# Kernel optimization log

Hardware: AMD Instinct MI355X
Metric: run time of the kernel (lower is better)

## Reference

```python
import jax, jax.numpy as jnp
import numpy as np

B, F, S = 64, 128, 2048
K_LIST = [8, 4, 2]  # c**i for i in range(k,0,-1) with k=3, c=2
EPS = 1e-5


def setup_inputs() -> dict:
    key = jax.random.key(0)
    ks = jax.random.split(key, 16)
    d = {}
    d["x"] = jax.random.normal(ks[0], (B, F, S), dtype=jnp.float32)
    # BatchNorm1d(seq_len*feature_num) affine params (train-mode batch stats)
    d["bn_gamma"] = jnp.ones((F * S,), jnp.float32)
    d["bn_beta"] = jnp.zeros((F * S,), jnp.float32)
    i = 1
    for s, k in enumerate(K_LIST):
        L = S // k
        d[f"selw1_{s}"] = (jax.random.normal(ks[i], (3 * F, 64), jnp.float32) / np.sqrt(3 * F)).astype(jnp.float32); i += 1
        d[f"selb1_{s}"] = jnp.zeros((64,), jnp.float32)
        d[f"selw2_{s}"] = (jax.random.normal(ks[i], (64, 1), jnp.float32) / 8.0).astype(jnp.float32); i += 1
        d[f"selb2_{s}"] = jnp.zeros((1,), jnp.float32)
        d[f"linw1_{s}"] = (jax.random.normal(ks[i], (L, L), jnp.float32) / np.sqrt(L)).astype(jnp.float32); i += 1
        d[f"linb1_{s}"] = jnp.zeros((L,), jnp.float32)
        d[f"linw2_{s}"] = (jax.random.normal(ks[i], (L, 2 * L), jnp.float32) / np.sqrt(L)).astype(jnp.float32); i += 1
        d[f"linb2_{s}"] = jnp.zeros((2 * L,), jnp.float32)
    return d


def _forward(x, bn_gamma, bn_beta, sel, lin):
    Bx, Fx, Sx = x.shape
    # BatchNorm1d over flattened [B, F*S] channels, training-mode batch stats (biased var)
    xf = x.reshape(Bx, -1)
    mu = xf.mean(axis=0)
    var = xf.var(axis=0)
    xf = (xf - mu) * jax.lax.rsqrt(var + EPS) * bn_gamma + bn_beta
    x = xf.reshape(Bx, Fx, Sx)

    samples = []
    for s, k in enumerate(K_LIST):
        L = Sx // k
        xr = x.reshape(Bx, Fx, L, k)           # non-overlapping windows (kernel==stride)
        avg = xr.mean(axis=-1)                 # AvgPool1d  [B, F, L]
        mx = xr.max(axis=-1)                   # MaxPool1d  [B, F, L]
        pfs = 0.5 * (avg + mx)
        stats = jnp.concatenate(
            [pfs.mean(axis=-1), pfs.std(axis=-1, ddof=1), pfs.max(axis=-1)], axis=1
        )                                      # [B, 3F]
        w1, b1, w2, b2 = sel[s]
        w = jax.nn.sigmoid(jax.nn.relu(stats @ w1 + b1) @ w2 + b2)  # [B, 1] (dropout is eval/identity)
        w = w[:, :, None]                      # [B, 1, 1]
        samples.append(w * avg + (1.0 - w) * mx)
    samples.append(x)

    for s in range(len(K_LIST)):
        lw1, lb1, lw2, lb2 = lin[s]
        h = jax.nn.gelu(samples[s] @ lw1 + lb1, approximate=False)
        samples[s + 1] = samples[s + 1] + h @ lw2 + lb2
    return samples[-1]


def reference(x, bn_gamma, bn_beta,
              selw1_0, selb1_0, selw2_0, selb2_0, linw1_0, linb1_0, linw2_0, linb2_0,
              selw1_1, selb1_1, selw2_1, selb2_1, linw1_1, linb1_1, linw2_1, linb2_1,
              selw1_2, selb1_2, selw2_2, selb2_2, linw1_2, linb1_2, linw2_2, linb2_2):
    sel = [(selw1_0, selb1_0, selw2_0, selb2_0),
           (selw1_1, selb1_1, selw2_1, selb2_1),
           (selw1_2, selb1_2, selw2_2, selb2_2)]
    lin = [(linw1_0, linb1_0, linw2_0, linb2_0),
           (linw1_1, linb1_1, linw2_1, linb2_1),
           (linw1_2, linb1_2, linw2_2, linb2_2)]
    return _forward(x, bn_gamma, bn_beta, sel, lin)
```

## Files before the change

kernel.cpp:

```cpp
#include <hip/hip_runtime.h>
#include <hip/hip_bf16.h>
#include <math.h>

#define B_ 64
#define F_ 128
#define S_ 2048
#define FS_ (F_*S_)
#define M_  (B_*F_)
#define EPS_ 1e-5f

typedef __bf16 v8bf __attribute__((ext_vector_type(8)));
typedef float  v16f __attribute__((ext_vector_type(16)));

__device__ __forceinline__ unsigned short f2bf_rne(float f) {
  unsigned int u = __float_as_uint(f);
  u += 0x7FFF + ((u >> 16) & 1);
  return (unsigned short)(u >> 16);
}
__device__ __forceinline__ float b2f(unsigned short u) {
  return __uint_as_float(((unsigned int)u) << 16);
}
__device__ __forceinline__ unsigned int pack2(float a, float b) {
  return (unsigned int)f2bf_rne(a) | ((unsigned int)f2bf_rne(b) << 16);
}

__device__ __forceinline__ float gelu_exact(float x) {
  return 0.5f * x * (1.0f + erff(x * 0.70710678118654752f));
}

#define GLDS16(g, l) __builtin_amdgcn_global_load_lds( \
    (const __attribute__((address_space(1))) unsigned int*)(g), \
    (__attribute__((address_space(3))) unsigned int*)(l), 16, 0, 0)

__global__ __launch_bounds__(256) void bn_stats_k(const float* __restrict__ x,
    const float* __restrict__ gamma, const float* __restrict__ beta,
    float* __restrict__ scl, float* __restrict__ shf)
{
  int j4 = blockIdx.x * 256 + threadIdx.x;
  const float4* x4 = (const float4*)x;
  float sum[4] = {0,0,0,0}, sq[4] = {0,0,0,0};
  for (int b = 0; b < B_; b++) {
    float4 v = x4[(size_t)b * (FS_/4) + j4];
    float vv[4] = {v.x, v.y, v.z, v.w};
    #pragma unroll
    for (int i = 0; i < 4; i++) { sum[i] += vv[i]; sq[i] += vv[i]*vv[i]; }
  }
  #pragma unroll
  for (int i = 0; i < 4; i++) {
    int j = j4*4 + i;
    float mu  = sum[i] * (1.0f/B_);
    float var = sq[i] * (1.0f/B_) - mu*mu;
    float rstd = rsqrtf(var + EPS_);
    float g = gamma[j];
    scl[j] = rstd * g;
    shf[j] = beta[j] - mu * rstd * g;
  }
}

__global__ __launch_bounds__(256) void bnpool_k(const float* __restrict__ x,
    const float* __restrict__ scl, const float* __restrict__ shf,
    unsigned short* __restrict__ xnb, float* __restrict__ stats)
{
  int bf = blockIdx.x, t = threadIdx.x;
  int b = bf >> 7, f = bf & 127;
  const float4* xp  = (const float4*)(x   + (size_t)bf * S_);
  const float4* scp = (const float4*)(scl + (size_t)f  * S_);
  const float4* shp = (const float4*)(shf + (size_t)f  * S_);

  float xr[8];
  #pragma unroll
  for (int h = 0; h < 2; h++) {
    int i4 = t*2 + h;
    float4 v = xp[i4], sc = scp[i4], sh = shp[i4];
    xr[h*4+0] = fmaf(v.x, sc.x, sh.x);
    xr[h*4+1] = fmaf(v.y, sc.y, sh.y);
    xr[h*4+2] = fmaf(v.z, sc.z, sh.z);
    xr[h*4+3] = fmaf(v.w, sc.w, sh.w);
  }
  uint4 pk;
  pk.x = pack2(xr[0], xr[1]); pk.y = pack2(xr[2], xr[3]);
  pk.z = pack2(xr[4], xr[5]); pk.w = pack2(xr[6], xr[7]);
  ((uint4*)(xnb + (size_t)bf * S_))[t] = pk;

  float a2[4], m2[4];
  float ps2 = 0.f, pq2 = 0.f, pm2 = -INFINITY;
  #pragma unroll
  for (int j = 0; j < 4; j++) {
    a2[j] = xr[2*j] + xr[2*j+1];
    m2[j] = fmaxf(xr[2*j], xr[2*j+1]);
    float pf = 0.5f * (0.5f * a2[j] + m2[j]);
    ps2 += pf; pq2 += pf*pf; pm2 = fmaxf(pm2, pf);
  }
  float a4[2], m4[2];
  float ps1 = 0.f, pq1 = 0.f, pm1 = -INFINITY;
  #pragma unroll
  for (int j = 0; j < 2; j++) {
    a4[j] = a2[2*j] + a2[2*j+1];
    m4[j] = fmaxf(m2[2*j], m2[2*j+1]);
    float pf = 0.5f * (0.25f * a4[j] + m4[j]);
    ps1 += pf; pq1 += pf*pf; pm1 = fmaxf(pm1, pf);
  }
  float a8 = a4[0] + a4[1];
  float m8 = fmaxf(m4[0], m4[1]);
  float pf8 = 0.5f * (0.125f * a8 + m8);
  float ps0 = pf8, pq0 = pf8*pf8, pm0 = pf8;

  __shared__ float wred[12];
  int lane = t & 63, wid = t >> 6;
  float PS[3] = {ps0, ps1, ps2}, PQ[3] = {pq0, pq1, pq2}, PM[3] = {pm0, pm1, pm2};
  int   LL[3] = {256, 512, 1024};
  #pragma unroll
  for (int s = 0; s < 3; s++) {
    float vs = PS[s], vq = PQ[s], vm = PM[s];
    #pragma unroll
    for (int off = 32; off > 0; off >>= 1) {
      vs += __shfl_down(vs, off);
      vq += __shfl_down(vq, off);
      vm = fmaxf(vm, __shfl_down(vm, off));
    }
    if (lane == 0) { wred[wid*3+0] = vs; wred[wid*3+1] = vq; wred[wid*3+2] = vm; }
    __syncthreads();
    if (t == 0) {
      float S = 0.f, Q = 0.f, Mx = -INFINITY;
      #pragma unroll
      for (int i = 0; i < 4; i++) {
        S += wred[i*3+0]; Q += wred[i*3+1]; Mx = fmaxf(Mx, wred[i*3+2]);
      }
      float L = (float)LL[s];
      float mean = S / L;
      float var  = (Q - S*S/L) / (L - 1.0f);
      float* base = stats + s*(64*384) + b*384;
      base[f]       = mean;
      base[128 + f] = sqrtf(fmaxf(var, 0.0f));
      base[256 + f] = Mx;
    }
    __syncthreads();
  }
}

__global__ __launch_bounds__(64) void selall_k(const float* __restrict__ stats,
    const float* w1_0, const float* b1_0, const float* w2_0, const float* b2_0,
    const float* w1_1, const float* b1_1, const float* w2_1, const float* b2_1,
    const float* w1_2, const float* b1_2, const float* w2_2, const float* b2_2,
    float* __restrict__ wsel)
{
  int s = blockIdx.y, b = blockIdx.x, j = threadIdx.x;
  const float *w1, *b1, *w2, *b2;
  if      (s == 0) { w1 = w1_0; b1 = b1_0; w2 = w2_0; b2 = b2_0; }
  else if (s == 1) { w1 = w1_1; b1 = b1_1; w2 = w2_1; b2 = b2_1; }
  else             { w1 = w1_2; b1 = b1_2; w2 = w2_2; b2 = b2_2; }
  const float* st = stats + s*(64*384) + b*384;
  float acc = b1[j];
  for (int i = 0; i < 384; i++) acc = fmaf(st[i], w1[i*64 + j], acc);
  float h = fmaxf(acc, 0.0f);
  float v = h * w2[j];
  for (int off = 32; off > 0; off >>= 1) v += __shfl_down(v, off);
  if (j == 0) wsel[s*64 + b] = 1.0f / (1.0f + expf(-(v + b2[0])));
}

__global__ __launch_bounds__(256) void combfused_k(const unsigned short* __restrict__ xnb,
    const float* __restrict__ wsel,
    unsigned short* __restrict__ o8, unsigned short* __restrict__ o4,
    unsigned short* __restrict__ o2)
{
  int bf = blockIdx.x, t = threadIdx.x, b = bf >> 7;
  float wA = wsel[b];
  float wB = wsel[64 + b];
  float wC = wsel[128 + b];
  uint4 pk = ((const uint4*)(xnb + (size_t)bf * S_))[t];
  unsigned int pw[4] = {pk.x, pk.y, pk.z, pk.w};
  float xr[8];
  #pragma unroll
  for (int h = 0; h < 4; h++) {
    xr[2*h]   = b2f((unsigned short)(pw[h] & 0xFFFF));
    xr[2*h+1] = b2f((unsigned short)(pw[h] >> 16));
  }
  float a2[4], m2[4];
  ushort4 u4o;
  unsigned short uu[4];
  #pragma unroll
  for (int j = 0; j < 4; j++) {
    a2[j] = xr[2*j] + xr[2*j+1];
    m2[j] = fmaxf(xr[2*j], xr[2*j+1]);
    uu[j] = f2bf_rne(wC * (0.5f * a2[j]) + (1.0f - wC) * m2[j]);
  }
  u4o.x = uu[0]; u4o.y = uu[1]; u4o.z = uu[2]; u4o.w = uu[3];
  ((ushort4*)(o2 + (size_t)bf * 1024))[t] = u4o;

  float a4[2], m4[2];
  ushort2 u2o;
  #pragma unroll
  for (int j = 0; j < 2; j++) {
    a4[j] = a2[2*j] + a2[2*j+1];
    m4[j] = fmaxf(m2[2*j], m2[2*j+1]);
    unsigned short uv = f2bf_rne(wB * (0.25f * a4[j]) + (1.0f - wB) * m4[j]);
    if (j == 0) u2o.x = uv; else u2o.y = uv;
  }
  ((ushort2*)(o4 + (size_t)bf * 512))[t] = u2o;

  float a8 = a4[0] + a4[1];
  float m8 = fmaxf(m4[0], m4[1]);
  o8[(size_t)bf * 256 + t] = f2bf_rne(wA * (0.125f * a8) + (1.0f - wA) * m8);
}

__global__ __launch_bounds__(256) void wt_all_k(
    const float* w10, unsigned short* t10,
    const float* w20, unsigned short* t20,
    const float* w11, unsigned short* t11,
    const float* w21, unsigned short* t21,
    const float* w12, unsigned short* t12,
    const float* w22, unsigned short* t22)
{
  int bx = blockIdx.x;
  const float* W; unsigned short* T; int K, N, loc;
  if      (bx < 64)   { W = w10; T = t10; K = 256;  N = 256;  loc = bx; }
  else if (bx < 192)  { W = w20; T = t20; K = 256;  N = 512;  loc = bx - 64; }
  else if (bx < 448)  { W = w11; T = t11; K = 512;  N = 512;  loc = bx - 192; }
  else if (bx < 960)  { W = w21; T = t21; K = 512;  N = 1024; loc = bx - 448; }
  else if (bx < 1984) { W = w12; T = t12; K = 1024; N = 1024; loc = bx - 960; }
  else                { W = w22; T = t22; K = 1024; N = 2048; loc = bx - 1984; }
  int nx = N >> 5;
  int k0 = (loc / nx) << 5;
  int n0 = (loc % nx) << 5;
  __shared__ float tile[32][33];
  int tx = threadIdx.x & 31, ty = threadIdx.x >> 5;
  #pragma unroll
  for (int i = ty; i < 32; i += 8)
    tile[i][tx] = W[(size_t)(k0 + i) * N + n0 + tx];
  __syncthreads();
  #pragma unroll
  for (int i = ty; i < 32; i += 8)
    T[(size_t)(n0 + i) * K + k0 + tx] = f2bf_rne(tile[tx][i]);
}

template<int MODE, int TM>
__global__ __launch_bounds__(256) void mgemm_k(
    const unsigned short* __restrict__ A,
    const unsigned short* __restrict__ Wt,
    const float* __restrict__ bias,
    const unsigned short* Cold,
    unsigned short* Obf,
    float* Of32,
    int K, int N)
{
  constexpr int MI = TM / 64;
  constexpr int RA = TM / 4;
  __shared__ v8bf As8[TM * 8];
  __shared__ v8bf Bs8[128 * 8];
  const int tid  = threadIdx.x;
  const int lane = tid & 63;
  const int w    = tid >> 6;
  const int bm   = blockIdx.y * TM;
  const int bn   = blockIdx.x * 128;
  const int wm   = (w >> 1) * (TM / 2);
  const int wn   = (w & 1) * 64;

  v16f acc[MI][2];
  #pragma unroll
  for (int i = 0; i < MI; i++)
    #pragma unroll
    for (int j = 0; j < 2; j++)
      #pragma unroll
      for (int r = 0; r < 16; r++) acc[i][j][r] = 0.f;

  const int lrow = lane >> 3;
  const int lchk = (lane & 7) ^ lrow;
  const unsigned short* ag = A  + (size_t)(bm + w*RA + lrow) * K + lchk * 8;
  const unsigned short* bg = Wt + (size_t)(bn + w*32 + lrow) * K + lchk * 8;
  char* al = (char*)As8 + w*RA*128;
  char* bl = (char*)Bs8 + w*32*128;
  const size_t row8 = (size_t)8 * K;

  for (int k0 = 0; k0 < K; k0 += 64) {
    __syncthreads();
    #pragma unroll
    for (int q = 0; q < RA/8; q++)
      GLDS16(ag + q*row8 + k0, al + q*8*128);
    #pragma unroll
    for (int q = 0; q < 4; q++)
      GLDS16(bg + q*row8 + k0, bl + q*8*128);
    __syncthreads();

    #pragma unroll
    for (int s = 0; s < 4; s++) {
      const int c = 2*s + (lane >> 5);
      const int slot = c ^ (lane & 7);
      v8bf af[MI], bfr[2];
      #pragma unroll
      for (int i = 0; i < MI; i++)
        af[i] = As8[(wm + i*32 + (lane & 31))*8 + slot];
      #pragma unroll
      for (int j = 0; j < 2; j++)
        bfr[j] = Bs8[(wn + j*32 + (lane & 31))*8 + slot];
      #pragma unroll
      for (int i = 0; i < MI; i++)
        #pragma unroll
        for (int j = 0; j < 2; j++)
          acc[i][j] = __builtin_amdgcn_mfma_f32_32x32x16_bf16(af[i], bfr[j], acc[i][j], 0, 0, 0);
    }
  }

  const int col0 = bn + wn + (lane & 31);
  const int rb0  = bm + wm + ((lane >> 5) << 2);
  #pragma unroll
  for (int j = 0; j < 2; j++) {
    int c = col0 + j*32;
    float bv = bias[c];
    #pragma unroll
    for (int i = 0; i < MI; i++) {
      #pragma unroll
      for (int r = 0; r < 16; r++) {
        int rr = rb0 + i*32 + (r & 3) + ((r >> 2) << 3);
        size_t idx = (size_t)rr * N + c;
        float t = acc[i][j][r] + bv;
        if (MODE == 0) {
          Obf[idx] = f2bf_rne(gelu_exact(t));
        } else if (MODE == 1) {
          Obf[idx] = f2bf_rne(t + b2f(Cold[idx]));
        } else {
          Of32[idx] = t + b2f(Cold[idx]);
        }
      }
    }
  }
}

extern "C" void kernel_launch(void* const* d_in, const int* in_sizes, int n_in,
                              void* d_out, int out_size, void* d_ws, size_t ws_size,
                              hipStream_t stream)
{
  const float* x     = (const float*)d_in[0];
  const float* gamma = (const float*)d_in[1];
  const float* beta  = (const float*)d_in[2];
  float* out = (float*)d_out;
  float* ws  = (float*)d_ws;

  static const int KS[3] = {8, 4, 2};

  size_t off = 0;
  float* scl   = ws + off; off += FS_;
  float* shf   = ws + off; off += FS_;
  float* stats = ws + off; off += 3*64*384;
  float* wsel  = ws + off; off += 256;
  unsigned short* xnb = (unsigned short*)(ws + off); off += (size_t)M_ * S_ / 2;
  unsigned short* sampb[3];
  sampb[0] = (unsigned short*)(ws + off); off += (size_t)M_ * 256 / 2;
  sampb[1] = (unsigned short*)(ws + off); off += (size_t)M_ * 512 / 2;
  sampb[2] = (unsigned short*)(ws + off); off += (size_t)M_ * 1024 / 2;
  unsigned short* hb = (unsigned short*)(ws + off); off += (size_t)M_ * 2048 / 2;
  unsigned short *wt1[3], *wt2[3];
  for (int s = 0; s < 3; s++) {
    int L = S_ / KS[s];
    wt1[s] = (unsigned short*)(ws + off); off += (size_t)L * L / 2;
    wt2[s] = (unsigned short*)(ws + off); off += (size_t)L * 2 * L / 2;
  }

  wt_all_k<<<4032, 256, 0, stream>>>(
      (const float*)d_in[3 + 0*8 + 4], wt1[0], (const float*)d_in[3 + 0*8 + 6], wt2[0],
      (const float*)d_in[3 + 1*8 + 4], wt1[1], (const float*)d_in[3 + 1*8 + 6], wt2[1],
      (const float*)d_in[3 + 2*8 + 4], wt1[2], (const float*)d_in[3 + 2*8 + 6], wt2[2]);

  bn_stats_k<<<FS_/4/256, 256, 0, stream>>>(x, gamma, beta, scl, shf);
  bnpool_k<<<M_, 256, 0, stream>>>(x, scl, shf, xnb, stats);
  selall_k<<<dim3(64, 3), 64, 0, stream>>>(stats,
      (const float*)d_in[3+0], (const float*)d_in[4+0], (const float*)d_in[5+0], (const float*)d_in[6+0],
      (const float*)d_in[3+8], (const float*)d_in[4+8], (const float*)d_in[5+8], (const float*)d_in[6+8],
      (const float*)d_in[3+16], (const float*)d_in[4+16], (const float*)d_in[5+16], (const float*)d_in[6+16],
      wsel);
  combfused_k<<<M_, 256, 0, stream>>>(xnb, wsel, sampb[0], sampb[1], sampb[2]);

  mgemm_k<0,64><<<dim3(2, 128), 256, 0, stream>>>(
      sampb[0], wt1[0], (const float*)d_in[3+0*8+5], nullptr, hb, nullptr, 256, 256);
  mgemm_k<1,64><<<dim3(4, 128), 256, 0, stream>>>(
      hb, wt2[0], (const float*)d_in[3+0*8+7], sampb[1], sampb[1], nullptr, 256, 512);
  mgemm_k<0,64><<<dim3(4, 128), 256, 0, stream>>>(
      sampb[1], wt1[1], (const float*)d_in[3+1*8+5], nullptr, hb, nullptr, 512, 512);
  mgemm_k<1,64><<<dim3(8, 128), 256, 0, stream>>>(
      hb, wt2[1], (const float*)d_in[3+1*8+7], sampb[2], sampb[2], nullptr, 512, 1024);
  mgemm_k<0,64><<<dim3(8, 128), 256, 0, stream>>>(
      sampb[2], wt1[2], (const float*)d_in[3+2*8+5], nullptr, hb, nullptr, 1024, 1024);
  mgemm_k<2,128><<<dim3(16, 64), 256, 0, stream>>>(
      hb, wt2[2], (const float*)d_in[3+2*8+7], xnb, nullptr, out, 1024, 2048);
}
```

Measured before the change: 372.0 us.

## Prefetch next GEMM K-tile into registers while computing current tile

Replaces the direct global-to-LDS loads in the bf16 MFMA GEMM with register prefetching. The next K-tile is loaded into registers while the MFMAs run on the current tile, then written to LDS after a barrier. This aims to hide global memory latency behind compute without adding LDS buffers. The cost is extra VGPR pressure and a register round-trip for the data.

```diff
diff --git a/kernel.cpp b/kernel.cpp
--- a/kernel.cpp
+++ b/kernel.cpp
@@ -27,10 +27,6 @@
 __device__ __forceinline__ float gelu_exact(float x) {
   return 0.5f * x * (1.0f + erff(x * 0.70710678118654752f));
 }
-
-#define GLDS16(g, l) __builtin_amdgcn_global_load_lds( \
-    (const __attribute__((address_space(1))) unsigned int*)(g), \
-    (__attribute__((address_space(3))) unsigned int*)(l), 16, 0, 0)
 
 __global__ __launch_bounds__(256) void bn_stats_k(const float* __restrict__ x,
     const float* __restrict__ gamma, const float* __restrict__ beta,
@@ -245,6 +241,7 @@
 {
   constexpr int MI = TM / 64;
   constexpr int RA = TM / 4;
+  constexpr int QA = RA / 8;
   __shared__ v8bf As8[TM * 8];
   __shared__ v8bf Bs8[128 * 8];
   const int tid  = threadIdx.x;
@@ -267,20 +264,31 @@
   const int lchk = (lane & 7) ^ lrow;
   const unsigned short* ag = A  + (size_t)(bm + w*RA + lrow) * K + lchk * 8;
   const unsigned short* bg = Wt + (size_t)(bn + w*32 + lrow) * K + lchk * 8;
-  char* al = (char*)As8 + w*RA*128;
-  char* bl = (char*)Bs8 + w*32*128;
+  v8bf* alw = As8 + w*RA*8 + lane;
+  v8bf* blw = Bs8 + w*32*8 + lane;
   const size_t row8 = (size_t)8 * K;
 
-  for (int k0 = 0; k0 < K; k0 += 64) {
+  uint4 pa[QA], pb[4];
+  #pragma unroll
+  for (int q = 0; q < QA; q++) pa[q] = *(const uint4*)(ag + q*row8);
+  #pragma unroll
+  for (int q = 0; q < 4;  q++) pb[q] = *(const uint4*)(bg + q*row8);
+  #pragma unroll
+  for (int q = 0; q < QA; q++) alw[q*64] = *(const v8bf*)&pa[q];
+  #pragma unroll
+  for (int q = 0; q < 4;  q++) blw[q*64] = *(const v8bf*)&pb[q];
+
+  const int ntile = K >> 6;
+  for (int it = 0; it < ntile; it++) {
     __syncthreads();
-    #pragma unroll
-    for (int q = 0; q < RA/8; q++)
-      GLDS16(ag + q*row8 + k0, al + q*8*128);
-    #pragma unroll
-    for (int q = 0; q < 4; q++)
-      GLDS16(bg + q*row8 + k0, bl + q*8*128);
-    __syncthreads();
-
+    const bool more = (it + 1 < ntile);
+    const int k1 = (it + 1) << 6;
+    if (more) {
+      #pragma unroll
+      for (int q = 0; q < QA; q++) pa[q] = *(const uint4*)(ag + q*row8 + k1);
+      #pragma unroll
+      for (int q = 0; q < 4;  q++) pb[q] = *(const uint4*)(bg + q*row8 + k1);
+    }
     #pragma unroll
     for (int s = 0; s < 4; s++) {
       const int c = 2*s + (lane >> 5);
@@ -297,6 +305,13 @@
         #pragma unroll
         for (int j = 0; j < 2; j++)
           acc[i][j] = __builtin_amdgcn_mfma_f32_32x32x16_bf16(af[i], bfr[j], acc[i][j], 0, 0, 0);
+    }
+    __syncthreads();
+    if (more) {
+      #pragma unroll
+      for (int q = 0; q < QA; q++) alw[q*64] = *(const v8bf*)&pa[q];
+      #pragma unroll
+      for (int q = 0; q < 4;  q++) blw[q*64] = *(const v8bf*)&pb[q];
     }
   }
 
```

After: 376.2 us. No clear change (+1.1%).
